# Performance work log

Measured on AMD Instinct MI355X. Metric: run time of the kernel, lower is better.

The kernel has to match this reference:

```python
import jax, jax.numpy as jnp
import numpy as np

N = 50000
E = 800000
F_IN = 256
HID = 64
HEADS = 4
CLASSES = 8
NEG_SLOPE = 0.2  # PyG GATConv default


def setup_inputs() -> dict:
    key = jax.random.key(0)
    ks = jax.random.split(key, 10)
    x = jax.random.normal(ks[0], (N, F_IN), jnp.float32)
    edge_index = jax.random.randint(ks[1], (2, E), 0, N, dtype=jnp.int32)
    # layer 1: feature -> hidden, heads=4, concat
    W1 = jax.random.normal(ks[2], (F_IN, HEADS * HID), jnp.float32) / np.sqrt(F_IN).astype(np.float32)
    att1_src = jax.random.normal(ks[3], (HEADS, HID), jnp.float32) / np.sqrt(HID).astype(np.float32)
    att1_dst = jax.random.normal(ks[4], (HEADS, HID), jnp.float32) / np.sqrt(HID).astype(np.float32)
    b1 = jnp.zeros((HEADS * HID,), jnp.float32)
    # layer 2: hidden*heads -> classes, heads=1
    W2 = jax.random.normal(ks[5], (HEADS * HID, CLASSES), jnp.float32) / np.sqrt(HEADS * HID).astype(np.float32)
    att2_src = jax.random.normal(ks[6], (1, CLASSES), jnp.float32) / np.sqrt(CLASSES).astype(np.float32)
    att2_dst = jax.random.normal(ks[7], (1, CLASSES), jnp.float32) / np.sqrt(CLASSES).astype(np.float32)
    b2 = jnp.zeros((CLASSES,), jnp.float32)
    return {"x": x, "edge_index": edge_index, "W1": W1, "att1_src": att1_src,
            "att1_dst": att1_dst, "b1": b1, "W2": W2, "att2_src": att2_src,
            "att2_dst": att2_dst, "b2": b2}


def _gat_conv(x, W, a_src, a_dst, b, src, dst, heads, ch, n):
    # h: [N, H, C] per-head projected features
    h = (x @ W).reshape(n, heads, ch)
    alpha_src = jnp.einsum('nhc,hc->nh', h, a_src)  # [N, H]
    alpha_dst = jnp.einsum('nhc,hc->nh', h, a_dst)  # [N, H]
    # per-edge attention logits (gather along edges)
    e = jax.nn.leaky_relu(alpha_src[src] + alpha_dst[dst], NEG_SLOPE)  # [E, H]
    # segment softmax over edges sharing a destination node
    e_max = jax.ops.segment_max(e, dst, num_segments=n)  # [N, H]
    ex = jnp.exp(e - e_max[dst])
    denom = jax.ops.segment_sum(ex, dst, num_segments=n)  # [N, H]
    alpha = ex / denom[dst]  # self-loops guarantee denom > 0
    # weighted scatter-sum of source messages
    out = jax.ops.segment_sum(alpha[..., None] * h[src], dst, num_segments=n)  # [N, H, C]
    return out.reshape(n, heads * ch) + b


def reference(x, edge_index, W1, att1_src, att1_dst, b1, W2, att2_src, att2_dst, b2):
    n = x.shape[0]
    # PyG GATConv adds self-loops by default
    loop = jnp.arange(n, dtype=edge_index.dtype)
    src = jnp.concatenate([edge_index[0], loop])
    dst = jnp.concatenate([edge_index[1], loop])
    h = _gat_conv(x, W1, att1_src, att1_dst, b1, src, dst, HEADS, HID, n)
    h = jax.nn.relu(h)
    # dropout is identity in eval mode (training=self.training)
    out = _gat_conv(h, W2, att2_src, att2_dst, b2, src, dst, 1, CLASSES, n)
    return jax.nn.log_softmax(out, axis=1)
```

## Files before the change

kernel.cpp:

```cpp
#include <hip/hip_runtime.h>
#include <math.h>

#define NNODES 50000
#define NEDGES 800000
#define ETOT   850000
#define SLOPE  0.2f
#define BSLOTS 96

typedef unsigned short ushort_t;
typedef unsigned int   uint_t;
typedef __attribute__((ext_vector_type(8))) __bf16 bf16x8;
typedef __attribute__((ext_vector_type(4))) float  floatx4;

__device__ __forceinline__ float leaky(float v) { return fmaxf(v, SLOPE * v); }

__device__ __forceinline__ ushort_t f2bf(float f) {
    uint_t u = __float_as_uint(f);
    uint_t r = (u + 0x7fffu + ((u >> 16) & 1u)) >> 16;
    return (ushort_t)r;
}
__device__ __forceinline__ float lof(uint_t u) { return __uint_as_float(u << 16); }
__device__ __forceinline__ float hif(uint_t u) { return __uint_as_float(u & 0xffff0000u); }

__device__ __forceinline__ float hsel(float4 v, int h) {
    float t0 = (h & 1) ? v.y : v.x;
    float t1 = (h & 1) ? v.w : v.z;
    return (h & 2) ? t1 : t0;
}

__device__ __forceinline__ int esrc(const int* ei, int e) { return e < NEDGES ? ei[e]          : e - NEDGES; }
__device__ __forceinline__ int edst(const int* ei, int e) { return e < NEDGES ? ei[NEDGES + e] : e - NEDGES; }

__global__ void prep_k(const int* __restrict__ ei, int* __restrict__ cnt,
                       int* __restrict__ bkt,
                       const float* __restrict__ W1, ushort_t* __restrict__ W1c,
                       const float* __restrict__ b1, const float* __restrict__ W2,
                       float* __restrict__ b1p, float* __restrict__ W2p) {
    int bid = blockIdx.x, tid = threadIdx.x;
    if (bid < 256) {
        int i = bid * 256 + tid;
        int k = i >> 8, n = i & 255;
        W1c[(k >> 5) * 8192 + n * 32 + (k & 31)] = f2bf(W1[i]);
    } else if (bid == 256) {
        int chp = tid;
        int q = chp & 63, c = q >> 2, t = q & 3;
        int ch = (chp & 192) | (t * 16 + c);
        b1p[chp] = b1[ch];
        #pragma unroll
        for (int j = 0; j < 8; ++j) W2p[chp * 8 + j] = W2[ch * 8 + j];
    }
    int e = bid * 256 + tid;
    if (e < ETOT) {
        int d = edst(ei, e), s = esrc(ei, e);
        int pos = atomicAdd(&cnt[d], 1);
        if (pos < BSLOTS) bkt[d * BSLOTS + pos] = s;
    }
}

__global__ __launch_bounds__(256) void gemm1_k(const float* __restrict__ X,
                                               const ushort_t* __restrict__ W1c,
                                               const float* __restrict__ att_s,
                                               const float* __restrict__ att_d,
                                               ushort_t* __restrict__ h1b,
                                               float* __restrict__ as1,
                                               float* __restrict__ ad1, int M) {
    __shared__ ushort_t Als[64 * 40];
    __shared__ ushort_t Bls[256 * 40];
    int tid = threadIdx.x;
    int row0 = blockIdx.x * 64;
    int wv = tid >> 6, lane = tid & 63, c15 = lane & 15, quad = lane >> 4;
    floatx4 acc[4][4] = {};

    for (int kc = 0; kc < 8; ++kc) {
        __syncthreads();
        {
            int r = tid >> 3, c4 = tid & 7;
            #pragma unroll
            for (int p = 0; p < 2; ++p) {
                int rr = r + p * 32;
                int row = row0 + rr;
                float4 v = make_float4(0.f, 0.f, 0.f, 0.f);
                if (row < M) v = *(const float4*)&X[(size_t)row * 256 + kc * 32 + c4 * 4];
                uint2 pk;
                pk.x = (uint_t)f2bf(v.x) | ((uint_t)f2bf(v.y) << 16);
                pk.y = (uint_t)f2bf(v.z) | ((uint_t)f2bf(v.w) << 16);
                *(uint2*)&Als[rr * 40 + c4 * 4] = pk;
            }
        }
        {
            const uint4* srcp = (const uint4*)(W1c + kc * 8192);
            #pragma unroll
            for (int c = 0; c < 4; ++c) {
                int el = tid + c * 256;
                uint4 v = srcp[el];
                int n = el >> 2, kk8 = (el & 3) * 8;
                *(uint4*)&Bls[n * 40 + kk8] = v;
            }
        }
        __syncthreads();
        uint4 af[4], bfr[4];
        #pragma unroll
        for (int t = 0; t < 4; ++t)
            af[t] = *(const uint4*)&Als[(t * 16 + c15) * 40 + quad * 8];
        #pragma unroll
        for (int t = 0; t < 4; ++t)
            bfr[t] = *(const uint4*)&Bls[(wv * 64 + t * 16 + c15) * 40 + quad * 8];
        #pragma unroll
        for (int tm = 0; tm < 4; ++tm)
            #pragma unroll
            for (int tn = 0; tn < 4; ++tn)
                acc[tm][tn] = __builtin_amdgcn_mfma_f32_16x16x32_bf16(
                    __builtin_bit_cast(bf16x8, af[tm]),
                    __builtin_bit_cast(bf16x8, bfr[tn]),
                    acc[tm][tn], 0, 0, 0);
    }

    float asv[4], adv[4];
    #pragma unroll
    for (int tn = 0; tn < 4; ++tn) {
        asv[tn] = att_s[wv * 64 + tn * 16 + c15];
        adv[tn] = att_d[wv * 64 + tn * 16 + c15];
    }
    float ps[4][4], pd[4][4];
    #pragma unroll
    for (int tm = 0; tm < 4; ++tm)
        #pragma unroll
        for (int r = 0; r < 4; ++r) {
            float vs = 0.f, vd = 0.f;
            #pragma unroll
            for (int tn = 0; tn < 4; ++tn) {
                float a = acc[tm][tn][r];
                vs += a * asv[tn]; vd += a * adv[tn];
            }
            ps[tm][r] = vs; pd[tm][r] = vd;
        }
    #pragma unroll
    for (int tm = 0; tm < 4; ++tm) {
        #pragma unroll
        for (int r = 0; r < 4; ++r) {
            int row = row0 + tm * 16 + quad * 4 + r;
            if (row < M) {
                uint2 pk;
                pk.x = (uint_t)f2bf(acc[tm][0][r]) | ((uint_t)f2bf(acc[tm][1][r]) << 16);
                pk.y = (uint_t)f2bf(acc[tm][2][r]) | ((uint_t)f2bf(acc[tm][3][r]) << 16);
                *(uint2*)&h1b[(size_t)row * 256 + wv * 64 + c15 * 4] = pk;
            }
        }
    }
    #pragma unroll
    for (int off = 1; off < 16; off <<= 1)
        #pragma unroll
        for (int tm = 0; tm < 4; ++tm)
            #pragma unroll
            for (int r = 0; r < 4; ++r) {
                ps[tm][r] += __shfl_xor(ps[tm][r], off, 64);
                pd[tm][r] += __shfl_xor(pd[tm][r], off, 64);
            }
    if (c15 == 0) {
        #pragma unroll
        for (int tm = 0; tm < 4; ++tm)
            #pragma unroll
            for (int r = 0; r < 4; ++r) {
                int row = row0 + tm * 16 + quad * 4 + r;
                if (row < M) {
                    as1[row * 4 + wv] = ps[tm][r];
                    ad1[row * 4 + wv] = pd[tm][r];
                }
            }
    }
}

__global__ __launch_bounds__(256) void f1_k(const int* __restrict__ cnt,
                                            const int* __restrict__ bkt,
                                            const float* __restrict__ as1,
                                            const float* __restrict__ ad1,
                                            const ushort_t* __restrict__ h1b,
                                            const float* __restrict__ b1p,
                                            const float* __restrict__ W2p,
                                            const float* __restrict__ a2sw,
                                            const float* __restrict__ a2dw,
                                            float* __restrict__ h2,
                                            float* __restrict__ a2s,
                                            float* __restrict__ a2d) {
    int wv = threadIdx.x >> 6;
    int lane = threadIdx.x & 63;
    int half = lane >> 5, l32 = lane & 31;
    int node = blockIdx.x * 8 + wv * 2 + half;
    int h = l32 >> 3;
    int deg = min(cnt[node], BSLOTS);
    const int* bp = bkt + (size_t)node * BSLOTS;
    float4 advec = *(const float4*)&ad1[(size_t)node * 4];
    __shared__ float wls[4][2][32][4];

    float acc[8] = {};
    float dn0, dn1, dn2, dn3;
    if (deg <= 32) {
        bool act = l32 < deg;
        int s_reg = node;
        if (act) s_reg = bp[l32];
        float4 av = *(const float4*)&as1[(size_t)s_reg * 4];
        float e0 = act ? __expf(leaky(av.x + advec.x)) : 0.f;
        float e1 = act ? __expf(leaky(av.y + advec.y)) : 0.f;
        float e2 = act ? __expf(leaky(av.z + advec.z)) : 0.f;
        float e3 = act ? __expf(leaky(av.w + advec.w)) : 0.f;
        *(float4*)&wls[wv][half][l32][0] = make_float4(e0, e1, e2, e3);
        dn0 = e0; dn1 = e1; dn2 = e2; dn3 = e3;
        #pragma unroll
        for (int off = 16; off; off >>= 1) {
            dn0 += __shfl_xor(dn0, off, 64);
            dn1 += __shfl_xor(dn1, off, 64);
            dn2 += __shfl_xor(dn2, off, 64);
            dn3 += __shfl_xor(dn3, off, 64);
        }
        int nb = (deg + 15) & ~15;
        int sbase = half << 5;
        for (int base = 0; base < nb; base += 16) {
            #pragma unroll
            for (int u = 0; u < 16; ++u) {
                int e = base + u;
                int se = __shfl(s_reg, sbase + e, 64);
                float w = wls[wv][half][e][h];
                uint4 v = *(const uint4*)&h1b[(size_t)se * 256 + l32 * 8];
                acc[0] += w * lof(v.x); acc[1] += w * hif(v.x);
                acc[2] += w * lof(v.y); acc[3] += w * hif(v.y);
                acc[4] += w * lof(v.z); acc[5] += w * hif(v.z);
                acc[6] += w * lof(v.w); acc[7] += w * hif(v.w);
            }
        }
    } else {
        dn0 = dn1 = dn2 = dn3 = 0.f;
        for (int j = l32; j < deg; j += 32) {
            int s = bp[j];
            float4 av = *(const float4*)&as1[(size_t)s * 4];
            dn0 += __expf(leaky(av.x + advec.x));
            dn1 += __expf(leaky(av.y + advec.y));
            dn2 += __expf(leaky(av.z + advec.z));
            dn3 += __expf(leaky(av.w + advec.w));
        }
        #pragma unroll
        for (int off = 16; off; off >>= 1) {
            dn0 += __shfl_xor(dn0, off, 64);
            dn1 += __shfl_xor(dn1, off, 64);
            dn2 += __shfl_xor(dn2, off, 64);
            dn3 += __shfl_xor(dn3, off, 64);
        }
        float advh = hsel(advec, h);
        int cmax = deg - 1;
        for (int base = 0; base < deg; base += 8) {
            #pragma unroll
            for (int u = 0; u < 8; ++u) {
                int e = base + u;
                int ce = min(e, cmax);
                int se = bp[ce];
                float ash = as1[(size_t)se * 4 + h];
                float w = (e < deg) ? __expf(leaky(ash + advh)) : 0.f;
                uint4 v = *(const uint4*)&h1b[(size_t)se * 256 + l32 * 8];
                acc[0] += w * lof(v.x); acc[1] += w * hif(v.x);
                acc[2] += w * lof(v.y); acc[3] += w * hif(v.y);
                acc[4] += w * lof(v.z); acc[5] += w * hif(v.z);
                acc[6] += w * lof(v.w); acc[7] += w * hif(v.w);
            }
        }
    }
    float rdh = 1.f / hsel(make_float4(dn0, dn1, dn2, dn3), h);
    #pragma unroll
    for (int c = 0; c < 8; ++c) acc[c] *= rdh;

    int k0 = l32 * 8;
    float4 ba = *(const float4*)&b1p[k0];
    float4 bb = *(const float4*)&b1p[k0 + 4];
    float xv[8];
    xv[0] = fmaxf(acc[0] + ba.x, 0.f); xv[1] = fmaxf(acc[1] + ba.y, 0.f);
    xv[2] = fmaxf(acc[2] + ba.z, 0.f); xv[3] = fmaxf(acc[3] + ba.w, 0.f);
    xv[4] = fmaxf(acc[4] + bb.x, 0.f); xv[5] = fmaxf(acc[5] + bb.y, 0.f);
    xv[6] = fmaxf(acc[6] + bb.z, 0.f); xv[7] = fmaxf(acc[7] + bb.w, 0.f);
    float p[8] = {};
    #pragma unroll
    for (int q = 0; q < 8; ++q) {
        const float4* w2p = (const float4*)&W2p[(size_t)(k0 + q) * 8];
        float4 wa = w2p[0], wb = w2p[1];
        p[0] += xv[q] * wa.x; p[1] += xv[q] * wa.y; p[2] += xv[q] * wa.z; p[3] += xv[q] * wa.w;
        p[4] += xv[q] * wb.x; p[5] += xv[q] * wb.y; p[6] += xv[q] * wb.z; p[7] += xv[q] * wb.w;
    }
    #pragma unroll
    for (int off = 16; off; off >>= 1)
        #pragma unroll
        for (int c = 0; c < 8; ++c) p[c] += __shfl_xor(p[c], off, 64);
    if (l32 == 0) {
        *(float4*)&h2[(size_t)node * 8]     = make_float4(p[0], p[1], p[2], p[3]);
        *(float4*)&h2[(size_t)node * 8 + 4] = make_float4(p[4], p[5], p[6], p[7]);
        float vs = 0.f, vd = 0.f;
        #pragma unroll
        for (int c = 0; c < 8; ++c) { vs += p[c] * a2sw[c]; vd += p[c] * a2dw[c]; }
        a2s[node] = vs; a2d[node] = vd;
    }
}

__global__ __launch_bounds__(256) void f2_k(const int* __restrict__ cnt,
                                            const int* __restrict__ bkt,
                                            const float* __restrict__ a2s,
                                            const float* __restrict__ a2d,
                                            const float* __restrict__ h2,
                                            const float* __restrict__ b2,
                                            float* __restrict__ out) {
    int wv = threadIdx.x >> 6;
    int lane = threadIdx.x & 63;
    int half = lane >> 5, l32 = lane & 31;
    int node = blockIdx.x * 8 + wv * 2 + half;
    int deg = min(cnt[node], BSLOTS);
    const int* bp = bkt + (size_t)node * BSLOTS;
    float adv = a2d[node];

    float acc = 0.f;
    float den;
    int c = l32 & 7, eg = l32 >> 3;
    if (deg <= 32) {
        bool act = l32 < deg;
        int s_reg = node;
        if (act) s_reg = bp[l32];
        float ex = act ? __expf(leaky(a2s[s_reg] + adv)) : 0.f;
        den = ex;
        #pragma unroll
        for (int off = 16; off; off >>= 1) den += __shfl_xor(den, off, 64);
        int nb = (deg + 3) & ~3;
        int sbase = half << 5;
        for (int base = 0; base < nb; base += 4) {
            int e = base + eg;
            int se = __shfl(s_reg, sbase + e, 64);
            float w  = __shfl(ex,    sbase + e, 64);
            acc += w * h2[(size_t)se * 8 + c];
        }
    } else {
        den = 0.f;
        for (int j = l32; j < deg; j += 32) {
            int s = bp[j];
            den += __expf(leaky(a2s[s] + adv));
        }
        #pragma unroll
        for (int off = 16; off; off >>= 1) den += __shfl_xor(den, off, 64);
        int cmax = deg - 1;
        for (int base = 0; base < deg; base += 4) {
            int e = base + eg, ce = min(e, cmax);
            int se = bp[ce];
            float w = (e < deg) ? __expf(leaky(a2s[se] + adv)) : 0.f;
            acc += w * h2[(size_t)se * 8 + c];
        }
    }
    acc += __shfl_xor(acc, 8, 64);
    acc += __shfl_xor(acc, 16, 64);
    acc /= den;

    float v = acc + b2[c];
    float mx = v;
    #pragma unroll
    for (int off = 1; off < 8; off <<= 1) mx = fmaxf(mx, __shfl_xor(mx, off, 64));
    float ex2 = __expf(v - mx);
    float ss = ex2;
    #pragma unroll
    for (int off = 1; off < 8; off <<= 1) ss += __shfl_xor(ss, off, 64);
    if (l32 < 8) out[(size_t)node * 8 + c] = v - (mx + __logf(ss));
}

extern "C" void kernel_launch(void* const* d_in, const int* in_sizes, int n_in,
                              void* d_out, int out_size, void* d_ws, size_t ws_size,
                              hipStream_t stream) {
    const float* x    = (const float*)d_in[0];
    const int*   ei   = (const int*)  d_in[1];
    const float* W1   = (const float*)d_in[2];
    const float* a1sw = (const float*)d_in[3];
    const float* a1dw = (const float*)d_in[4];
    const float* b1   = (const float*)d_in[5];
    const float* W2   = (const float*)d_in[6];
    const float* a2sw = (const float*)d_in[7];
    const float* a2dw = (const float*)d_in[8];
    const float* b2   = (const float*)d_in[9];
    float* out = (float*)d_out;

    ushort_t* h1b = (ushort_t*)d_ws;
    ushort_t* W1c = h1b + 12800000;
    float* as1  = (float*)(W1c + 65536);
    float* ad1  = as1 + 200000;
    float* h2   = ad1 + 200000;
    float* a2s  = h2  + 400000;
    float* a2d  = a2s + 50000;
    float* b1p  = a2d + 50000;
    float* W2p  = b1p + 256;
    int*   cnt  = (int*)(W2p + 2048);
    int*   bkt  = cnt + 50000;

    hipMemsetAsync(cnt, 0, (size_t)50000 * sizeof(int), stream);
    prep_k<<<(ETOT + 255) / 256, 256, 0, stream>>>(ei, cnt, bkt, W1, W1c, b1, W2, b1p, W2p);

    gemm1_k<<<(NNODES + 63) / 64, 256, 0, stream>>>(x, W1c, a1sw, a1dw, h1b, as1, ad1, NNODES);

    f1_k<<<NNODES / 8, 256, 0, stream>>>(cnt, bkt, as1, ad1, h1b, b1p, W2p,
                                         a2sw, a2dw, h2, a2s, a2d);

    f2_k<<<NNODES / 8, 256, 0, stream>>>(cnt, bkt, a2s, a2d, h2, b2, out);
}
```

Baseline: 303.1 us.

## Overlap edge bucketing with layer-1 GEMM in one launch and drop memset

Moves the edge-bucketing atomics out of the prep kernel and into extra blocks of the GEMM kernel, so the bucketing runs concurrently with the GEMM tiles. The count array is now zeroed inside prep_k instead of by a separate memset, which removes one launch. The unroll granularity of the aggregation loop for low-degree nodes drops from 16 to 8, so fewer padded edges are processed. Bucket order can still vary between runs because of the atomics, and the GEMM and bucketing blocks now compete for the same compute units.

```diff
diff --git a/kernel.cpp b/kernel.cpp
--- a/kernel.cpp
+++ b/kernel.cpp
@@ -6,6 +6,8 @@
 #define ETOT   850000
 #define SLOPE  0.2f
 #define BSLOTS 96
+#define NTILE  782
+#define BBLK   518
 
 typedef unsigned short ushort_t;
 typedef unsigned int   uint_t;
@@ -31,42 +33,49 @@
 __device__ __forceinline__ int esrc(const int* ei, int e) { return e < NEDGES ? ei[e]          : e - NEDGES; }
 __device__ __forceinline__ int edst(const int* ei, int e) { return e < NEDGES ? ei[NEDGES + e] : e - NEDGES; }
 
-__global__ void prep_k(const int* __restrict__ ei, int* __restrict__ cnt,
-                       int* __restrict__ bkt,
-                       const float* __restrict__ W1, ushort_t* __restrict__ W1c,
+__global__ void prep_k(const float* __restrict__ W1, ushort_t* __restrict__ W1c,
                        const float* __restrict__ b1, const float* __restrict__ W2,
-                       float* __restrict__ b1p, float* __restrict__ W2p) {
+                       float* __restrict__ b1p, float* __restrict__ W2p,
+                       int* __restrict__ cnt) {
     int bid = blockIdx.x, tid = threadIdx.x;
+    int gtid = bid * 256 + tid;
     if (bid < 256) {
-        int i = bid * 256 + tid;
-        int k = i >> 8, n = i & 255;
-        W1c[(k >> 5) * 8192 + n * 32 + (k & 31)] = f2bf(W1[i]);
+        int k = gtid >> 8, n = gtid & 255;
+        W1c[(k >> 5) * 8192 + n * 32 + (k & 31)] = f2bf(W1[gtid]);
     } else if (bid == 256) {
         int chp = tid;
-        int q = chp & 63, c = q >> 2, t = q & 3;
-        int ch = (chp & 192) | (t * 16 + c);
+        int q = chp & 63, cc = q >> 2, t = q & 3;
+        int ch = (chp & 192) | (t * 16 + cc);
         b1p[chp] = b1[ch];
         #pragma unroll
         for (int j = 0; j < 8; ++j) W2p[chp * 8 + j] = W2[ch * 8 + j];
     }
-    int e = bid * 256 + tid;
-    if (e < ETOT) {
-        int d = edst(ei, e), s = esrc(ei, e);
-        int pos = atomicAdd(&cnt[d], 1);
-        if (pos < BSLOTS) bkt[d * BSLOTS + pos] = s;
-    }
-}
-
-__global__ __launch_bounds__(256) void gemm1_k(const float* __restrict__ X,
-                                               const ushort_t* __restrict__ W1c,
-                                               const float* __restrict__ att_s,
-                                               const float* __restrict__ att_d,
-                                               ushort_t* __restrict__ h1b,
-                                               float* __restrict__ as1,
-                                               float* __restrict__ ad1, int M) {
+    if (gtid < NNODES) cnt[gtid] = 0;
+}
+
+__global__ __launch_bounds__(256) void gb_k(const float* __restrict__ X,
+                                            const ushort_t* __restrict__ W1c,
+                                            const float* __restrict__ att_s,
+                                            const float* __restrict__ att_d,
+                                            ushort_t* __restrict__ h1b,
+                                            float* __restrict__ as1,
+                                            float* __restrict__ ad1,
+                                            const int* __restrict__ ei,
+                                            int* __restrict__ cnt,
+                                            int* __restrict__ bkt) {
     __shared__ ushort_t Als[64 * 40];
     __shared__ ushort_t Bls[256 * 40];
     int tid = threadIdx.x;
+
+    if (blockIdx.x >= NTILE) {
+        for (int e = (blockIdx.x - NTILE) * 256 + tid; e < ETOT; e += BBLK * 256) {
+            int d = edst(ei, e), s = esrc(ei, e);
+            int pos = atomicAdd(&cnt[d], 1);
+            if (pos < BSLOTS) bkt[d * BSLOTS + pos] = s;
+        }
+        return;
+    }
+
     int row0 = blockIdx.x * 64;
     int wv = tid >> 6, lane = tid & 63, c15 = lane & 15, quad = lane >> 4;
     floatx4 acc[4][4] = {};
@@ -80,7 +89,7 @@
                 int rr = r + p * 32;
                 int row = row0 + rr;
                 float4 v = make_float4(0.f, 0.f, 0.f, 0.f);
-                if (row < M) v = *(const float4*)&X[(size_t)row * 256 + kc * 32 + c4 * 4];
+                if (row < NNODES) v = *(const float4*)&X[(size_t)row * 256 + kc * 32 + c4 * 4];
                 uint2 pk;
                 pk.x = (uint_t)f2bf(v.x) | ((uint_t)f2bf(v.y) << 16);
                 pk.y = (uint_t)f2bf(v.z) | ((uint_t)f2bf(v.w) << 16);
@@ -139,7 +148,7 @@
         #pragma unroll
         for (int r = 0; r < 4; ++r) {
             int row = row0 + tm * 16 + quad * 4 + r;
-            if (row < M) {
+            if (row < NNODES) {
                 uint2 pk;
                 pk.x = (uint_t)f2bf(acc[tm][0][r]) | ((uint_t)f2bf(acc[tm][1][r]) << 16);
                 pk.y = (uint_t)f2bf(acc[tm][2][r]) | ((uint_t)f2bf(acc[tm][3][r]) << 16);
@@ -162,7 +171,7 @@
             #pragma unroll
             for (int r = 0; r < 4; ++r) {
                 int row = row0 + tm * 16 + quad * 4 + r;
-                if (row < M) {
+                if (row < NNODES) {
                     as1[row * 4 + wv] = ps[tm][r];
                     ad1[row * 4 + wv] = pd[tm][r];
                 }
@@ -212,11 +221,11 @@
             dn2 += __shfl_xor(dn2, off, 64);
             dn3 += __shfl_xor(dn3, off, 64);
         }
-        int nb = (deg + 15) & ~15;
+        int nb = (deg + 7) & ~7;
         int sbase = half << 5;
-        for (int base = 0; base < nb; base += 16) {
-            #pragma unroll
-            for (int u = 0; u < 16; ++u) {
+        for (int base = 0; base < nb; base += 8) {
+            #pragma unroll
+            for (int u = 0; u < 8; ++u) {
                 int e = base + u;
                 int se = __shfl(s_reg, sbase + e, 64);
                 float w = wls[wv][half][e][h];
@@ -388,10 +397,10 @@
     int*   cnt  = (int*)(W2p + 2048);
     int*   bkt  = cnt + 50000;
 
-    hipMemsetAsync(cnt, 0, (size_t)50000 * sizeof(int), stream);
-    prep_k<<<(ETOT + 255) / 256, 256, 0, stream>>>(ei, cnt, bkt, W1, W1c, b1, W2, b1p, W2p);
-
-    gemm1_k<<<(NNODES + 63) / 64, 256, 0, stream>>>(x, W1c, a1sw, a1dw, h1b, as1, ad1, NNODES);
+    prep_k<<<257, 256, 0, stream>>>(W1, W1c, b1, W2, b1p, W2p, cnt);
+
+    gb_k<<<NTILE + BBLK, 256, 0, stream>>>(x, W1c, a1sw, a1dw, h1b, as1, ad1,
+                                           ei, cnt, bkt);
 
     f1_k<<<NNODES / 8, 256, 0, stream>>>(cnt, bkt, as1, ad1, h1b, b1p, W2p,
                                          a2sw, a2dw, h2, a2s, a2d);
```

After: 286.1 us. 1.06x faster.
